# Kernel optimization log

Measured on AMD Instinct MI355X. Metric: run time of the kernel, lower is better.

## Reference

```python
import jax, jax.numpy as jnp
import numpy as np

N_NODES = 100000
N_EDGES = 1600000
N_GRAPHS = 128
IN_FEATS = 128
OUT_FEATS = 64


def setup_inputs() -> dict:
    key = jax.random.key(0)
    k1, k2, k3, k4, k5, k6 = jax.random.split(key, 6)
    features = jax.random.normal(k1, (N_NODES, IN_FEATS), jnp.float32)
    src = jax.random.randint(k2, (N_EDGES,), 0, N_NODES, dtype=jnp.int32)
    dst = jax.random.randint(k3, (N_EDGES,), 0, N_NODES, dtype=jnp.int32)
    graph_ids = jnp.sort(jax.random.randint(k4, (N_NODES,), 0, N_GRAPHS, dtype=jnp.int32))
    # Xavier-uniform init as in DGL GraphConv
    lim1 = float(np.sqrt(6.0 / (IN_FEATS + IN_FEATS)))
    lim2 = float(np.sqrt(6.0 / (IN_FEATS + OUT_FEATS)))
    W1 = jax.random.uniform(k5, (IN_FEATS, IN_FEATS), jnp.float32, -lim1, lim1)
    W2 = jax.random.uniform(k6, (IN_FEATS, OUT_FEATS), jnp.float32, -lim2, lim2)
    b1 = jnp.zeros((IN_FEATS,), jnp.float32)
    b2 = jnp.zeros((OUT_FEATS,), jnp.float32)
    return {"features": features, "W1": W1, "b1": b1, "W2": W2, "b2": b2,
            "src": src, "dst": dst, "graph_ids": graph_ids, "num_graphs": N_GRAPHS}


def _graph_conv(x, W, b, src, dst, n_nodes):
    # DGL GraphConv, norm='both': D_dst^{-1/2} A D_src^{-1/2} X W + b
    ones = jnp.ones(src.shape, x.dtype)
    deg_out = jax.ops.segment_sum(ones, src, num_segments=n_nodes)
    deg_in = jax.ops.segment_sum(ones, dst, num_segments=n_nodes)
    norm_src = jax.lax.rsqrt(jnp.maximum(deg_out, 1.0))  # [N]
    norm_dst = jax.lax.rsqrt(jnp.maximum(deg_in, 1.0))   # [N]
    h = (x * norm_src[:, None]) @ W                       # dense transform first
    agg = jax.ops.segment_sum(h[src], dst, num_segments=n_nodes)  # spmm-style scatter-add
    return agg * norm_dst[:, None] + b


def reference(features, W1, b1, W2, b2, src, dst, graph_ids, num_graphs):
    n = features.shape[0]
    h = jax.nn.relu(_graph_conv(features, W1, b1, src, dst, n))
    h = jax.nn.relu(_graph_conv(h, W2, b2, src, dst, n))
    # dgl.mean_nodes: per-graph mean over nodes
    sums = jax.ops.segment_sum(h, graph_ids, num_segments=num_graphs)
    counts = jax.ops.segment_sum(jnp.ones((n, 1), h.dtype), graph_ids, num_segments=num_graphs)
    return sums / jnp.maximum(counts, 1.0)
```

## Files before the change

kernel.cpp:

```cpp
#include <hip/hip_runtime.h>
#include <hip/hip_bf16.h>


#define NPP_SHIFT 9
#define NPP 512
#define MAXP 256
#define NB 512

typedef __attribute__((ext_vector_type(8))) short frag8;
typedef __attribute__((ext_vector_type(4))) float f32x4;

__launch_bounds__(256)
__global__ void passA_count(const int* __restrict__ src, const int* __restrict__ dst,
                            int E, int P, int* __restrict__ counts_src,
                            int* __restrict__ counts_dst) {
    __shared__ int h1[MAXP], h2[MAXP];
    int tid = threadIdx.x;
    for (int i = tid; i < P; i += 256) { h1[i] = 0; h2[i] = 0; }
    __syncthreads();
    int per_block = (E + NB - 1) / NB;
    int e0 = blockIdx.x * per_block;
    int e1 = min(e0 + per_block, E);
    for (int e = e0 + tid; e < e1; e += 256) {
        atomicAdd(&h1[src[e] >> NPP_SHIFT], 1);
        atomicAdd(&h2[dst[e] >> NPP_SHIFT], 1);
    }
    __syncthreads();
    for (int i = tid; i < P; i += 256) {
        counts_src[(size_t)blockIdx.x * P + i] = h1[i];
        counts_dst[(size_t)blockIdx.x * P + i] = h2[i];
    }
}

__launch_bounds__(1024)
__global__ void scanB(const int* __restrict__ counts, int* __restrict__ offs,
                      int* __restrict__ ptot, int P) {
    __shared__ int s[1024];
    int tid = threadIdx.x;
    int p = blockIdx.x % P;
    int st = blockIdx.x / P;
    const int* c = counts + (size_t)st * NB * P;
    int v = (tid < NB) ? c[(size_t)tid * P + p] : 0;
    s[tid] = v;
    __syncthreads();
    for (int off = 1; off < 1024; off <<= 1) {
        int t = (tid >= off) ? s[tid - off] : 0;
        __syncthreads();
        s[tid] += t;
        __syncthreads();
    }
    if (tid < NB) offs[(size_t)st * NB * P + (size_t)tid * P + p] = s[tid] - v;
    if (tid == 1023) ptot[st * P + p] = s[1023];
}

__launch_bounds__(512)
__global__ void scanP(const int* __restrict__ ptot, int* __restrict__ pbase, int P) {
    __shared__ int s[512];
    int tid = threadIdx.x;
    int seg = tid >> 8;
    int idx = tid & 255;
    int v = (idx < P) ? ptot[seg * P + idx] : 0;
    s[tid] = v;
    __syncthreads();
    for (int off = 1; off < 256; off <<= 1) {
        int t = (idx >= off) ? s[tid - off] : 0;
        __syncthreads();
        s[tid] += t;
        __syncthreads();
    }
    if (idx < P) pbase[seg * P + idx] = s[tid] - v;
}

__launch_bounds__(256)
__global__ void passC_scatter(const int* __restrict__ src, const int* __restrict__ dst,
                              int E, int P, const int* __restrict__ offs,
                              const int* __restrict__ pbase,
                              int* __restrict__ ebuf_src, int2* __restrict__ ebuf_dst) {
    __shared__ int cur1[MAXP], cur2[MAXP];
    int tid = threadIdx.x;
    for (int i = tid; i < P; i += 256) {
        cur1[i] = pbase[i] + offs[(size_t)blockIdx.x * P + i];
        cur2[i] = pbase[P + i] + offs[(size_t)NB * P + (size_t)blockIdx.x * P + i];
    }
    __syncthreads();
    int per_block = (E + NB - 1) / NB;
    int e0 = blockIdx.x * per_block;
    int e1 = min(e0 + per_block, E);
    for (int e = e0 + tid; e < e1; e += 256) {
        int s = src[e];
        int d = dst[e];
        int pos1 = atomicAdd(&cur1[s >> NPP_SHIFT], 1);
        ebuf_src[pos1] = s;
        int pos2 = atomicAdd(&cur2[d >> NPP_SHIFT], 1);
        ebuf_dst[pos2] = make_int2(d, s);
    }
}

__launch_bounds__(512)
__global__ void passD_build(const int* __restrict__ ebuf_src, const int2* __restrict__ ebuf_dst,
                            const int* __restrict__ ptot, const int* __restrict__ pbase,
                            float* __restrict__ norm_src, int* __restrict__ row_start,
                            int* __restrict__ csr_src, int N, int E, int P) {
    __shared__ int hs[NPP], hd[NPP], sc[NPP];
    int tid = threadIdx.x;
    int p = blockIdx.x;
    int node_lo = p << NPP_SHIFT;
    int nl = min(NPP, N - node_lo);
    hs[tid] = 0;
    hd[tid] = 0;
    __syncthreads();
    int nsrc = ptot[p];
    int base_s = pbase[p];
    for (int i = tid; i < nsrc; i += 512)
        atomicAdd(&hs[ebuf_src[base_s + i] - node_lo], 1);
    int ndst = ptot[P + p];
    int base_d = pbase[P + p];
    for (int i = tid; i < ndst; i += 512)
        atomicAdd(&hd[ebuf_dst[base_d + i].x - node_lo], 1);
    __syncthreads();
    if (tid < nl) norm_src[node_lo + tid] = rsqrtf((float)max(hs[tid], 1));
    int myh = hd[tid];
    sc[tid] = myh;
    __syncthreads();
    for (int off = 1; off < 512; off <<= 1) {
        int t = (tid >= off) ? sc[tid - off] : 0;
        __syncthreads();
        sc[tid] += t;
        __syncthreads();
    }
    int row0 = base_d + sc[tid] - myh;
    if (tid < nl) row_start[node_lo + tid] = row0;
    if (p == P - 1 && tid == 0) row_start[N] = E;
    __syncthreads();
    hd[tid] = row0;
    __syncthreads();
    for (int i = tid; i < ndst; i += 512) {
        int2 r = ebuf_dst[base_d + i];
        int pos = atomicAdd(&hd[r.x - node_lo], 1);
        csr_src[pos] = r.y;
    }
}

__global__ void gstart_kernel(const int* __restrict__ gids, int* __restrict__ g_start,
                              int n, int G) {
    int g = threadIdx.x;
    if (g > G) return;
    int lo = 0, hi = n;
    while (lo < hi) {
        int mid = (lo + hi) >> 1;
        if (gids[mid] < g) lo = mid + 1; else hi = mid;
    }
    g_start[g] = lo;
}

template <int COLS, bool BF16IN>
__launch_bounds__(256)
__global__ void gemm_mfma(const void* __restrict__ xin, const float* __restrict__ w,
                          const float* __restrict__ norm,
                          __hip_bfloat16* __restrict__ out, int n) {
    constexpr int NT = COLS / 16;
    __shared__ short wlds[4 * NT * 64 * 8];
    const int tid = threadIdx.x;
    for (int i = tid; i < 128 * COLS / 4; i += 256) {
        int k = (i * 4) / COLS;
        int n0 = (i * 4) % COLS;
        float4 wv = reinterpret_cast<const float4*>(w)[i];
        int c = k >> 5, q = (k >> 3) & 3, j = k & 7;
        float vals[4] = {wv.x, wv.y, wv.z, wv.w};
#pragma unroll
        for (int u = 0; u < 4; ++u) {
            int nn = n0 + u;
            int t = nn >> 4;
            int ln = (q << 4) | (nn & 15);
            union { __hip_bfloat16 b; short s; } cv;
            cv.b = __float2bfloat16(vals[u]);
            wlds[(((c * NT + t) << 6) | ln) * 8 + j] = cv.s;
        }
    }
    __syncthreads();

    const int lane = tid & 63;
    const int wid = tid >> 6;
    const int m = lane & 15;
    const int q = lane >> 4;
    const int ntiles = (n + 15) >> 4;
    const frag8* wfr = reinterpret_cast<const frag8*>(wlds);

    for (int wt = blockIdx.x * 4 + wid; wt < ntiles; wt += gridDim.x * 4) {
        const int row = (wt << 4) + m;
        frag8 af[4];
        if (row < n) {
            if constexpr (BF16IN) {
                const frag8* xp = reinterpret_cast<const frag8*>(
                    (const __hip_bfloat16*)xin + (size_t)row * 128);
#pragma unroll
                for (int c = 0; c < 4; ++c) af[c] = xp[c * 4 + q];
            } else {
                const float* xp = (const float*)xin + (size_t)row * 128;
                float nm = norm[row];
#pragma unroll
                for (int c = 0; c < 4; ++c) {
                    int base = c * 32 + q * 8;
                    float4 v0 = *reinterpret_cast<const float4*>(xp + base);
                    float4 v1 = *reinterpret_cast<const float4*>(xp + base + 4);
                    union { frag8 f; short s[8]; } a;
                    union { __hip_bfloat16 b; short s; } cv;
                    cv.b = __float2bfloat16(v0.x * nm); a.s[0] = cv.s;
                    cv.b = __float2bfloat16(v0.y * nm); a.s[1] = cv.s;
                    cv.b = __float2bfloat16(v0.z * nm); a.s[2] = cv.s;
                    cv.b = __float2bfloat16(v0.w * nm); a.s[3] = cv.s;
                    cv.b = __float2bfloat16(v1.x * nm); a.s[4] = cv.s;
                    cv.b = __float2bfloat16(v1.y * nm); a.s[5] = cv.s;
                    cv.b = __float2bfloat16(v1.z * nm); a.s[6] = cv.s;
                    cv.b = __float2bfloat16(v1.w * nm); a.s[7] = cv.s;
                    af[c] = a.f;
                }
            }
        } else {
#pragma unroll
            for (int c = 0; c < 4; ++c) af[c] = frag8{0, 0, 0, 0, 0, 0, 0, 0};
        }
        f32x4 acc[NT] = {};
#pragma unroll
        for (int c = 0; c < 4; ++c)
#pragma unroll
            for (int t = 0; t < NT; ++t)
                acc[t] = __builtin_amdgcn_mfma_f32_16x16x32_bf16(
                    af[c], wfr[(c * NT + t) * 64 + lane], acc[t], 0, 0, 0);
#pragma unroll
        for (int r = 0; r < 4; ++r) {
            int grow = (wt << 4) + q * 4 + r;
            if (grow < n) {
#pragma unroll
                for (int t = 0; t < NT; ++t)
                    out[(size_t)grow * COLS + t * 16 + m] = __float2bfloat16(acc[t][r]);
            }
        }
    }
}

__launch_bounds__(256)
__global__ void spmm1_kernel(const __hip_bfloat16* __restrict__ h,
                             const int* __restrict__ row_start,
                             const int* __restrict__ csr_src,
                             const float* __restrict__ b1,
                             const float* __restrict__ norm_src,
                             uint* __restrict__ out, int n) {
    int gw = (blockIdx.x * blockDim.x + threadIdx.x) >> 6;
    int lane = threadIdx.x & 63;
    if (gw >= n) return;
    int e0 = row_start[gw];
    int e1 = row_start[gw + 1];
    const uint* hp = reinterpret_cast<const uint*>(h);
    float2 acc = {0.f, 0.f};
    int e = e0;
    for (; e + 8 <= e1; e += 8) {
        uint v[8];
#pragma unroll
        for (int j = 0; j < 8; ++j)
            v[j] = hp[(size_t)csr_src[e + j] * 64 + lane];
#pragma unroll
        for (int j = 0; j < 8; ++j) {
            acc.x += __uint_as_float(v[j] << 16);
            acc.y += __uint_as_float(v[j] & 0xffff0000u);
        }
    }
    if (e + 4 <= e1) {
        uint v[4];
#pragma unroll
        for (int j = 0; j < 4; ++j)
            v[j] = hp[(size_t)csr_src[e + j] * 64 + lane];
#pragma unroll
        for (int j = 0; j < 4; ++j) {
            acc.x += __uint_as_float(v[j] << 16);
            acc.y += __uint_as_float(v[j] & 0xffff0000u);
        }
        e += 4;
    }
    if (e + 2 <= e1) {
        uint v0 = hp[(size_t)csr_src[e] * 64 + lane];
        uint v1 = hp[(size_t)csr_src[e + 1] * 64 + lane];
        acc.x += __uint_as_float(v0 << 16);
        acc.y += __uint_as_float(v0 & 0xffff0000u);
        acc.x += __uint_as_float(v1 << 16);
        acc.y += __uint_as_float(v1 & 0xffff0000u);
        e += 2;
    }
    if (e < e1) {
        uint v0 = hp[(size_t)csr_src[e] * 64 + lane];
        acc.x += __uint_as_float(v0 << 16);
        acc.y += __uint_as_float(v0 & 0xffff0000u);
    }
    float nd = rsqrtf((float)max(e1 - e0, 1));
    float ns = norm_src[gw];
    float2 bb = reinterpret_cast<const float2*>(b1)[lane];
    float ox = fmaxf(fmaf(acc.x, nd, bb.x), 0.f) * ns;
    float oy = fmaxf(fmaf(acc.y, nd, bb.y), 0.f) * ns;
    union { __hip_bfloat16 b; ushort s; } cx, cy;
    cx.b = __float2bfloat16(ox);
    cy.b = __float2bfloat16(oy);
    out[(size_t)gw * 64 + lane] = (uint)cx.s | ((uint)cy.s << 16);
}

__launch_bounds__(256)
__global__ void spmm2_kernel(const __hip_bfloat16* __restrict__ h,
                             const int* __restrict__ row_start,
                             const int* __restrict__ csr_src,
                             const float* __restrict__ b2, float* __restrict__ y, int n) {
    int gw = (blockIdx.x * blockDim.x + threadIdx.x) >> 6;
    int lane = threadIdx.x & 63;
    if (gw >= n) return;
    int e0 = row_start[gw];
    int e1 = row_start[gw + 1];
    const ushort* hp = reinterpret_cast<const ushort*>(h);
    float acc = 0.f;
    int e = e0;
    for (; e + 8 <= e1; e += 8) {
        uint v[8];
#pragma unroll
        for (int j = 0; j < 8; ++j)
            v[j] = hp[(size_t)csr_src[e + j] * 64 + lane];
#pragma unroll
        for (int j = 0; j < 8; ++j) acc += __uint_as_float(v[j] << 16);
    }
    if (e + 4 <= e1) {
        uint v[4];
#pragma unroll
        for (int j = 0; j < 4; ++j)
            v[j] = hp[(size_t)csr_src[e + j] * 64 + lane];
#pragma unroll
        for (int j = 0; j < 4; ++j) acc += __uint_as_float(v[j] << 16);
        e += 4;
    }
    if (e + 2 <= e1) {
        uint v0 = hp[(size_t)csr_src[e] * 64 + lane];
        uint v1 = hp[(size_t)csr_src[e + 1] * 64 + lane];
        acc += __uint_as_float(v0 << 16);
        acc += __uint_as_float(v1 << 16);
        e += 2;
    }
    if (e < e1) {
        uint v0 = hp[(size_t)csr_src[e] * 64 + lane];
        acc += __uint_as_float(v0 << 16);
    }
    float nd = rsqrtf((float)max(e1 - e0, 1));
    y[(size_t)gw * 64 + lane] = fmaxf(fmaf(acc, nd, b2[lane]), 0.f);
}

#define POOL_CHUNKS 8
__launch_bounds__(256)
__global__ void pool_kernel(const float* __restrict__ y, const int* __restrict__ g_start,
                            float* __restrict__ gsum) {
    int g = blockIdx.x / POOL_CHUNKS;
    int c = blockIdx.x % POOL_CHUNKS;
    int s = g_start[g];
    int e = g_start[g + 1];
    int lane = threadIdx.x & 63;
    int wave = threadIdx.x >> 6;
    float acc = 0.f;
    for (int i = s + c * 4 + wave; i < e; i += POOL_CHUNKS * 4) {
        acc += y[(size_t)i * 64 + lane];
    }
    __shared__ float sbuf[4][64];
    sbuf[wave][lane] = acc;
    __syncthreads();
    if (wave == 0) {
        float v = sbuf[0][lane] + sbuf[1][lane] + sbuf[2][lane] + sbuf[3][lane];
        atomicAdd(&gsum[(size_t)g * 64 + lane], v);
    }
}

__global__ void finalize_kernel(const float* __restrict__ gsum, const int* __restrict__ g_start,
                                float* __restrict__ out, int total) {
    int i = blockIdx.x * blockDim.x + threadIdx.x;
    if (i < total) {
        int g = i >> 6;
        float cnt = (float)(g_start[g + 1] - g_start[g]);
        out[i] = gsum[i] / fmaxf(cnt, 1.f);
    }
}

extern "C" void kernel_launch(void* const* d_in, const int* in_sizes, int n_in,
                              void* d_out, int out_size, void* d_ws, size_t ws_size,
                              hipStream_t stream) {
    const float* features = (const float*)d_in[0];
    const float* W1 = (const float*)d_in[1];
    const float* b1 = (const float*)d_in[2];
    const float* W2 = (const float*)d_in[3];
    const float* b2 = (const float*)d_in[4];
    const int* src = (const int*)d_in[5];
    const int* dst = (const int*)d_in[6];
    const int* gids = (const int*)d_in[7];
    const int N = in_sizes[7];
    const int E = in_sizes[5];
    const int G = out_size / 64;
    float* out = (float*)d_out;
    const int P = (N + NPP - 1) >> NPP_SHIFT;

    char* ws = (char*)d_ws;
    size_t off = 0;
    auto alloc = [&](size_t bytes) -> void* {
        void* p = ws + off;
        off = (off + bytes + 255) & ~(size_t)255;
        return p;
    };
    int* counts = (int*)alloc((size_t)2 * NB * P * 4);
    int* offs = (int*)alloc((size_t)2 * NB * P * 4);
    int* ptot = (int*)alloc((size_t)2 * P * 4);
    int* pbase = (int*)alloc((size_t)2 * P * 4);
    int* ebuf_src = (int*)alloc((size_t)E * 4);
    int2* ebuf_dst = (int2*)alloc((size_t)E * 8);
    float* norm_src = (float*)alloc((size_t)N * 4);
    int* row_start = (int*)alloc((size_t)(N + 1) * 4);
    int* csr_src = (int*)alloc((size_t)E * 4);
    int* g_start = (int*)alloc((size_t)(G + 1) * 4);
    float* gsum = (float*)alloc((size_t)G * 64 * 4);
    __hip_bfloat16* h1 = (__hip_bfloat16*)alloc((size_t)N * 128 * 2);
    __hip_bfloat16* x2n = (__hip_bfloat16*)alloc((size_t)N * 128 * 2);
    float* y = (float*)alloc((size_t)N * 64 * 4);
    __hip_bfloat16* h2 = h1;

    hipMemsetAsync(gsum, 0, (size_t)G * 64 * 4, stream);

    const int B = 256;
    passA_count<<<NB, 256, 0, stream>>>(src, dst, E, P, counts, counts + (size_t)NB * P);
    scanB<<<2 * P, 1024, 0, stream>>>(counts, offs, ptot, P);
    scanP<<<1, 512, 0, stream>>>(ptot, pbase, P);
    passC_scatter<<<NB, 256, 0, stream>>>(src, dst, E, P, offs, pbase, ebuf_src, ebuf_dst);
    passD_build<<<P, 512, 0, stream>>>(ebuf_src, ebuf_dst, ptot, pbase, norm_src, row_start,
                                       csr_src, N, E, P);
    gstart_kernel<<<1, 256, 0, stream>>>(gids, g_start, N, G);

    gemm_mfma<128, false><<<768, 256, 0, stream>>>(features, W1, norm_src, h1, N);
    spmm1_kernel<<<(N * 64 + B - 1) / B, B, 0, stream>>>(h1, row_start, csr_src, b1, norm_src,
                                                         (uint*)x2n, N);
    gemm_mfma<64, true><<<768, 256, 0, stream>>>(x2n, W2, nullptr, h2, N);
    spmm2_kernel<<<(N * 64 + B - 1) / B, B, 0, stream>>>(h2, row_start, csr_src, b2, y, N);
    pool_kernel<<<G * POOL_CHUNKS, 256, 0, stream>>>(y, g_start, gsum);
    finalize_kernel<<<(out_size + B - 1) / B, B, 0, stream>>>(gsum, g_start, out, out_size);
}
```

Measured before the change: 333.3 us.

## Fuse scan and pooling kernels, unroll SpMM gathers, store layer-2 output as bf16

The partition-base scan is folded into passC_scatter, with each block recomputing it redundantly. The graph-start search, memset, atomic pooling and finalize kernels are merged into a single pool kernel that binary-searches its bounds and writes the mean directly. The SpMM gather loops are unrolled to 16 edges to keep more loads in flight, and the spmm2 output is stored in bf16 to halve pooling traffic, at some cost in precision. Pooling now uses one block per graph instead of eight, which lowers parallelism in that stage.

```diff
diff --git a/kernel.cpp b/kernel.cpp
--- a/kernel.cpp
+++ b/kernel.cpp
@@ -53,34 +53,41 @@
     if (tid == 1023) ptot[st * P + p] = s[1023];
 }
 
-__launch_bounds__(512)
-__global__ void scanP(const int* __restrict__ ptot, int* __restrict__ pbase, int P) {
-    __shared__ int s[512];
-    int tid = threadIdx.x;
-    int seg = tid >> 8;
-    int idx = tid & 255;
-    int v = (idx < P) ? ptot[seg * P + idx] : 0;
-    s[tid] = v;
-    __syncthreads();
-    for (int off = 1; off < 256; off <<= 1) {
-        int t = (idx >= off) ? s[tid - off] : 0;
-        __syncthreads();
-        s[tid] += t;
-        __syncthreads();
-    }
-    if (idx < P) pbase[seg * P + idx] = s[tid] - v;
-}
-
 __launch_bounds__(256)
 __global__ void passC_scatter(const int* __restrict__ src, const int* __restrict__ dst,
                               int E, int P, const int* __restrict__ offs,
-                              const int* __restrict__ pbase,
+                              const int* __restrict__ ptot, int* __restrict__ pbase,
                               int* __restrict__ ebuf_src, int2* __restrict__ ebuf_dst) {
-    __shared__ int cur1[MAXP], cur2[MAXP];
+    __shared__ int cur1[MAXP], cur2[MAXP], sc[256];
     int tid = threadIdx.x;
-    for (int i = tid; i < P; i += 256) {
-        cur1[i] = pbase[i] + offs[(size_t)blockIdx.x * P + i];
-        cur2[i] = pbase[P + i] + offs[(size_t)NB * P + (size_t)blockIdx.x * P + i];
+    int v = (tid < P) ? ptot[tid] : 0;
+    sc[tid] = v;
+    __syncthreads();
+    for (int off = 1; off < 256; off <<= 1) {
+        int t = (tid >= off) ? sc[tid - off] : 0;
+        __syncthreads();
+        sc[tid] += t;
+        __syncthreads();
+    }
+    int base0 = sc[tid] - v;
+    if (tid < P) {
+        cur1[tid] = base0 + offs[(size_t)blockIdx.x * P + tid];
+        if (blockIdx.x == 0) pbase[tid] = base0;
+    }
+    __syncthreads();
+    v = (tid < P) ? ptot[P + tid] : 0;
+    sc[tid] = v;
+    __syncthreads();
+    for (int off = 1; off < 256; off <<= 1) {
+        int t = (tid >= off) ? sc[tid - off] : 0;
+        __syncthreads();
+        sc[tid] += t;
+        __syncthreads();
+    }
+    int base1 = sc[tid] - v;
+    if (tid < P) {
+        cur2[tid] = base1 + offs[(size_t)NB * P + (size_t)blockIdx.x * P + tid];
+        if (blockIdx.x == 0) pbase[P + tid] = base1;
     }
     __syncthreads();
     int per_block = (E + NB - 1) / NB;
@@ -139,18 +146,6 @@
         int pos = atomicAdd(&hd[r.x - node_lo], 1);
         csr_src[pos] = r.y;
     }
-}
-
-__global__ void gstart_kernel(const int* __restrict__ gids, int* __restrict__ g_start,
-                              int n, int G) {
-    int g = threadIdx.x;
-    if (g > G) return;
-    int lo = 0, hi = n;
-    while (lo < hi) {
-        int mid = (lo + hi) >> 1;
-        if (gids[mid] < g) lo = mid + 1; else hi = mid;
-    }
-    g_start[g] = lo;
 }
 
 template <int COLS, bool BF16IN>
@@ -254,7 +249,18 @@
     const uint* hp = reinterpret_cast<const uint*>(h);
     float2 acc = {0.f, 0.f};
     int e = e0;
-    for (; e + 8 <= e1; e += 8) {
+    for (; e + 16 <= e1; e += 16) {
+        uint v[16];
+#pragma unroll
+        for (int j = 0; j < 16; ++j)
+            v[j] = hp[(size_t)csr_src[e + j] * 64 + lane];
+#pragma unroll
+        for (int j = 0; j < 16; ++j) {
+            acc.x += __uint_as_float(v[j] << 16);
+            acc.y += __uint_as_float(v[j] & 0xffff0000u);
+        }
+    }
+    if (e + 8 <= e1) {
         uint v[8];
 #pragma unroll
         for (int j = 0; j < 8; ++j)
@@ -264,6 +270,7 @@
             acc.x += __uint_as_float(v[j] << 16);
             acc.y += __uint_as_float(v[j] & 0xffff0000u);
         }
+        e += 8;
     }
     if (e + 4 <= e1) {
         uint v[4];
@@ -306,7 +313,7 @@
 __global__ void spmm2_kernel(const __hip_bfloat16* __restrict__ h,
                              const int* __restrict__ row_start,
                              const int* __restrict__ csr_src,
-                             const float* __restrict__ b2, float* __restrict__ y, int n) {
+                             const float* __restrict__ b2, ushort* __restrict__ y, int n) {
     int gw = (blockIdx.x * blockDim.x + threadIdx.x) >> 6;
     int lane = threadIdx.x & 63;
     if (gw >= n) return;
@@ -315,13 +322,22 @@
     const ushort* hp = reinterpret_cast<const ushort*>(h);
     float acc = 0.f;
     int e = e0;
-    for (; e + 8 <= e1; e += 8) {
+    for (; e + 16 <= e1; e += 16) {
+        uint v[16];
+#pragma unroll
+        for (int j = 0; j < 16; ++j)
+            v[j] = hp[(size_t)csr_src[e + j] * 64 + lane];
+#pragma unroll
+        for (int j = 0; j < 16; ++j) acc += __uint_as_float(v[j] << 16);
+    }
+    if (e + 8 <= e1) {
         uint v[8];
 #pragma unroll
         for (int j = 0; j < 8; ++j)
             v[j] = hp[(size_t)csr_src[e + j] * 64 + lane];
 #pragma unroll
         for (int j = 0; j < 8; ++j) acc += __uint_as_float(v[j] << 16);
+        e += 8;
     }
     if (e + 4 <= e1) {
         uint v[4];
@@ -344,39 +360,48 @@
         acc += __uint_as_float(v0 << 16);
     }
     float nd = rsqrtf((float)max(e1 - e0, 1));
-    y[(size_t)gw * 64 + lane] = fmaxf(fmaf(acc, nd, b2[lane]), 0.f);
-}
-
-#define POOL_CHUNKS 8
-__launch_bounds__(256)
-__global__ void pool_kernel(const float* __restrict__ y, const int* __restrict__ g_start,
-                            float* __restrict__ gsum) {
-    int g = blockIdx.x / POOL_CHUNKS;
-    int c = blockIdx.x % POOL_CHUNKS;
-    int s = g_start[g];
-    int e = g_start[g + 1];
+    float val = fmaxf(fmaf(acc, nd, b2[lane]), 0.f);
+    union { __hip_bfloat16 b; ushort s; } cv;
+    cv.b = __float2bfloat16(val);
+    y[(size_t)gw * 64 + lane] = cv.s;
+}
+
+__launch_bounds__(256)
+__global__ void pool_kernel(const ushort* __restrict__ y, const int* __restrict__ gids,
+                            float* __restrict__ out, int n) {
+    int g = blockIdx.x;
+    int lo = 0, hi = n;
+    while (lo < hi) {
+        int mid = (lo + hi) >> 1;
+        if (gids[mid] < g) lo = mid + 1; else hi = mid;
+    }
+    int s = lo;
+    hi = n;
+    while (lo < hi) {
+        int mid = (lo + hi) >> 1;
+        if (gids[mid] < g + 1) lo = mid + 1; else hi = mid;
+    }
+    int e = lo;
     int lane = threadIdx.x & 63;
     int wave = threadIdx.x >> 6;
     float acc = 0.f;
-    for (int i = s + c * 4 + wave; i < e; i += POOL_CHUNKS * 4) {
-        acc += y[(size_t)i * 64 + lane];
-    }
+    int i = s + wave;
+    for (; i + 12 < e; i += 16) {
+        uint u0 = y[(size_t)(i + 0) * 64 + lane];
+        uint u1 = y[(size_t)(i + 4) * 64 + lane];
+        uint u2 = y[(size_t)(i + 8) * 64 + lane];
+        uint u3 = y[(size_t)(i + 12) * 64 + lane];
+        acc += __uint_as_float(u0 << 16) + __uint_as_float(u1 << 16) +
+               __uint_as_float(u2 << 16) + __uint_as_float(u3 << 16);
+    }
+    for (; i < e; i += 4)
+        acc += __uint_as_float((uint)y[(size_t)i * 64 + lane] << 16);
     __shared__ float sbuf[4][64];
     sbuf[wave][lane] = acc;
     __syncthreads();
     if (wave == 0) {
         float v = sbuf[0][lane] + sbuf[1][lane] + sbuf[2][lane] + sbuf[3][lane];
-        atomicAdd(&gsum[(size_t)g * 64 + lane], v);
-    }
-}
-
-__global__ void finalize_kernel(const float* __restrict__ gsum, const int* __restrict__ g_start,
-                                float* __restrict__ out, int total) {
-    int i = blockIdx.x * blockDim.x + threadIdx.x;
-    if (i < total) {
-        int g = i >> 6;
-        float cnt = (float)(g_start[g + 1] - g_start[g]);
-        out[i] = gsum[i] / fmaxf(cnt, 1.f);
+        out[(size_t)g * 64 + lane] = v / fmaxf((float)(e - s), 1.f);
     }
 }
 
@@ -413,29 +438,23 @@
     float* norm_src = (float*)alloc((size_t)N * 4);
     int* row_start = (int*)alloc((size_t)(N + 1) * 4);
     int* csr_src = (int*)alloc((size_t)E * 4);
-    int* g_start = (int*)alloc((size_t)(G + 1) * 4);
-    float* gsum = (float*)alloc((size_t)G * 64 * 4);
     __hip_bfloat16* h1 = (__hip_bfloat16*)alloc((size_t)N * 128 * 2);
     __hip_bfloat16* x2n = (__hip_bfloat16*)alloc((size_t)N * 128 * 2);
-    float* y = (float*)alloc((size_t)N * 64 * 4);
+    ushort* y = (ushort*)alloc((size_t)N * 64 * 2);
     __hip_bfloat16* h2 = h1;
-
-    hipMemsetAsync(gsum, 0, (size_t)G * 64 * 4, stream);
 
     const int B = 256;
     passA_count<<<NB, 256, 0, stream>>>(src, dst, E, P, counts, counts + (size_t)NB * P);
     scanB<<<2 * P, 1024, 0, stream>>>(counts, offs, ptot, P);
-    scanP<<<1, 512, 0, stream>>>(ptot, pbase, P);
-    passC_scatter<<<NB, 256, 0, stream>>>(src, dst, E, P, offs, pbase, ebuf_src, ebuf_dst);
+    passC_scatter<<<NB, 256, 0, stream>>>(src, dst, E, P, offs, ptot, pbase,
+                                          ebuf_src, ebuf_dst);
     passD_build<<<P, 512, 0, stream>>>(ebuf_src, ebuf_dst, ptot, pbase, norm_src, row_start,
                                        csr_src, N, E, P);
-    gstart_kernel<<<1, 256, 0, stream>>>(gids, g_start, N, G);
 
     gemm_mfma<128, false><<<768, 256, 0, stream>>>(features, W1, norm_src, h1, N);
     spmm1_kernel<<<(N * 64 + B - 1) / B, B, 0, stream>>>(h1, row_start, csr_src, b1, norm_src,
                                                          (uint*)x2n, N);
     gemm_mfma<64, true><<<768, 256, 0, stream>>>(x2n, W2, nullptr, h2, N);
     spmm2_kernel<<<(N * 64 + B - 1) / B, B, 0, stream>>>(h2, row_start, csr_src, b2, y, N);
-    pool_kernel<<<G * POOL_CHUNKS, 256, 0, stream>>>(y, g_start, gsum);
-    finalize_kernel<<<(out_size + B - 1) / B, B, 0, stream>>>(gsum, g_start, out, out_size);
-}
+    pool_kernel<<<G, 256, 0, stream>>>(y, gids, out, N);
+}
```

Result: no change. 331.8 us (-0.4%).
